# Performance work log

Measured on AMD Instinct MI355X. Metric: run time of the kernel, lower is better.

The kernel has to match this reference:

```python
import jax, jax.numpy as jnp
import numpy as np

S_SAMPLES = 8          # config.ray_samples_per_voxel
T_MIN = 1e-4           # early-termination transmittance threshold


def setup_inputs() -> dict:
    key = jax.random.key(0)
    kp, ks, kd, kc, km, ko, kr = jax.random.split(key, 7)
    V, N = 4096, 4096
    # voxel centers uniform in scene bounds [-1,1]^3
    positions = jax.random.uniform(kp, (V, 3), jnp.float32, -1.0, 1.0)
    # voxel edge lengths: small cubes
    sizes = jax.random.uniform(ks, (V,), jnp.float32, 0.02, 0.08)
    densities = jax.random.normal(kd, (V,), jnp.float32)  # raw, exp-activated
    colors = jax.random.normal(kc, (V, 27), jnp.float32)  # SH deg2: 9*3 coeffs
    morton_codes = jax.random.randint(km, (V,), 0, 16777216, jnp.int32)
    # camera at z=-3 with slight jitter, rays toward the scene
    ray_origins = jnp.tile(jnp.array([0.0, 0.0, -3.0], jnp.float32), (N, 1)) \
        + 0.01 * jax.random.normal(ko, (N, 3), jnp.float32)
    dirs = jax.random.uniform(kr, (N, 3), jnp.float32, -0.4, 0.4)
    dirs = dirs.at[:, 2].set(1.0)
    ray_directions = dirs / jnp.linalg.norm(dirs, axis=1, keepdims=True)
    return {"positions": positions, "sizes": sizes, "densities": densities,
            "colors": colors, "morton_codes": morton_codes,
            "ray_origins": ray_origins, "ray_directions": ray_directions}


def reference(positions, sizes, densities, colors, morton_codes,
              ray_origins, ray_directions):
    # ---- global morton + mean-ray-direction sort ----
    mean_d = ray_directions.mean(axis=0)                       # [3]
    dots = positions @ mean_d                                  # [V]
    keys = morton_codes.astype(jnp.float32) + dots * 1e-6
    order = jnp.argsort(keys)                                  # stable
    pos = positions[order]
    half = (sizes[order] * 0.5)[:, None]                       # [V,1]
    dens_act = jnp.exp(densities[order])                       # 'exp' activation
    col = jax.nn.sigmoid(colors[order][:, :3])                 # dc coeffs, sigmoid

    box_min = pos - half                                       # [V,3]
    box_max = pos + half

    # ---- per-ray slab AABB intersection (vectorized over rays x voxels) ----
    inv_dir = 1.0 / (ray_directions + 1e-8)                    # [N,3]
    o = ray_origins[:, None, :]                                # [N,1,3]
    t1 = (box_min[None, :, :] - o) * inv_dir[:, None, :]       # [N,V,3]
    t2 = (box_max[None, :, :] - o) * inv_dir[:, None, :]
    t_near = jnp.max(jnp.minimum(t1, t2), axis=-1)             # [N,V]
    t_far = jnp.min(jnp.maximum(t1, t2), axis=-1)
    valid = (t_near <= t_far) & (t_far > 0)
    tn = jnp.maximum(t_near, 0.0)

    # ---- per-ray stable sort by entry t (invalid pushed to +inf) ----
    sort_key = jnp.where(valid, tn, jnp.inf)
    idx = jnp.argsort(sort_key, axis=1)                        # [N,V], stable
    tn_s = jnp.take_along_axis(tn, idx, axis=1)
    tf_s = jnp.take_along_axis(t_far, idx, axis=1)
    valid_s = jnp.take_along_axis(valid, idx, axis=1)
    dens_s = dens_act[idx]                                     # [N,V]
    col_s = col[idx]                                           # [N,V,3]

    # ---- sequential alpha compositing via cumprod ----
    dt = (tf_s - tn_s) / S_SAMPLES
    op = 1.0 - jnp.exp(-dens_s * dt)
    op = jnp.where(valid_s, op, 0.0)                           # skipped voxels
    one_m = 1.0 - op
    T_before = jnp.concatenate(
        [jnp.ones_like(op[:, :1]), jnp.cumprod(one_m, axis=1)[:, :-1]], axis=1)
    active = T_before >= T_MIN                                 # early-break mask
    w = jnp.where(active, T_before * op, 0.0)                  # [N,V]

    rgb = jnp.einsum('nv,nvc->nc', w, col_s)                   # [N,3]
    depth = jnp.sum(w * (tn_s + tf_s) * 0.5, axis=1)           # mean of linspace
    final_T = jnp.prod(jnp.where(active, one_m, 1.0), axis=1)
    alpha = 1.0 - final_T
    return rgb, depth, alpha
```

## Files before the change

### kernel.cpp

```cpp
#include <hip/hip_runtime.h>
#include <hip/hip_bf16.h>

#define MAXH 64

__global__ __launch_bounds__(256) void vr_prep(
    const float* __restrict__ positions, const float* __restrict__ sizes,
    const float* __restrict__ densities, const float* __restrict__ colors,
    const int* __restrict__ morton, const float* __restrict__ ray_d,
    float4* __restrict__ P, float* __restrict__ K, float4* __restrict__ C,
    int V, int N)
{
    __shared__ float rx[256], ry[256], rz[256];
    int t = threadIdx.x;
    float sx = 0.f, sy = 0.f, sz = 0.f;
    for (int r = t; r < N; r += 256) {
        sx += ray_d[r*3+0]; sy += ray_d[r*3+1]; sz += ray_d[r*3+2];
    }
    rx[t] = sx; ry[t] = sy; rz[t] = sz;
    __syncthreads();
    for (int s = 128; s > 0; s >>= 1) {
        if (t < s) { rx[t] += rx[t+s]; ry[t] += ry[t+s]; rz[t] += rz[t+s]; }
        __syncthreads();
    }
    float inN = 1.0f / (float)N;
    float mdx = rx[0]*inN, mdy = ry[0]*inN, mdz = rz[0]*inN;

    int v = blockIdx.x * 256 + t;
    if (v < V) {
        float px = positions[v*3+0], py = positions[v*3+1], pz = positions[v*3+2];
        float h = sizes[v] * 0.5f;
        P[v] = make_float4(px, py, pz, h);
        K[v] = (float)morton[v] + (px*mdx + py*mdy + pz*mdz) * 1e-6f;
        float c0 = 1.0f/(1.0f + expf(-colors[v*27+0]));
        float c1 = 1.0f/(1.0f + expf(-colors[v*27+1]));
        float c2 = 1.0f/(1.0f + expf(-colors[v*27+2]));
        C[v] = make_float4(c0, c1, c2, expf(densities[v]));
    }
}

__global__ __launch_bounds__(256) void vr_render(
    const float4* __restrict__ P, const float* __restrict__ K,
    const float4* __restrict__ C,
    const float* __restrict__ ray_o, const float* __restrict__ ray_d,
    float* __restrict__ out, int V, int N)
{
    __shared__ float h_tn[4][MAXH], h_tf[4][MAXH], h_key[4][MAXH];
    __shared__ int   h_v[4][MAXH], s_ord[4][MAXH];
    __shared__ float p_op[4][MAXH], p_c0[4][MAXH], p_c1[4][MAXH],
                     p_c2[4][MAXH], p_mid[4][MAXH];
    __shared__ int   cntL[4];
    __shared__ float rp[4][9];

    int t    = threadIdx.x;
    int lane = t & 63;
    int w    = t >> 6;

    if (t < 4) {
        cntL[t] = 0;
        int ray = blockIdx.x * 4 + t;
        if (ray < N) {
            float ox = ray_o[ray*3+0], oy = ray_o[ray*3+1], oz = ray_o[ray*3+2];
            float dx = ray_d[ray*3+0], dy = ray_d[ray*3+1], dz = ray_d[ray*3+2];
            float ix = 1.0f/(dx + 1e-8f), iy = 1.0f/(dy + 1e-8f), iz = 1.0f/(dz + 1e-8f);
            rp[t][0] = ix;        rp[t][1] = iy;        rp[t][2] = iz;
            rp[t][3] = -ox*ix;    rp[t][4] = -oy*iy;    rp[t][5] = -oz*iz;
            rp[t][6] = fabsf(ix); rp[t][7] = fabsf(iy); rp[t][8] = fabsf(iz);
        } else {
            float qn = __int_as_float(0x7FC00000);
            #pragma unroll
            for (int j = 0; j < 9; ++j) rp[t][j] = qn;
        }
    }
    __syncthreads();

    float ixr[4], iyr[4], izr[4], nxr[4], nyr[4], nzr[4], axr[4], ayr[4], azr[4];
    #pragma unroll
    for (int r = 0; r < 4; ++r) {
        ixr[r] = rp[r][0]; iyr[r] = rp[r][1]; izr[r] = rp[r][2];
        nxr[r] = rp[r][3]; nyr[r] = rp[r][4]; nzr[r] = rp[r][5];
        axr[r] = rp[r][6]; ayr[r] = rp[r][7]; azr[r] = rp[r][8];
    }

    for (int v0 = t; v0 < V; v0 += 512) {
        int v1 = v0 + 256;
        float4 pa = P[v0];
        float4 pb = (v1 < V) ? P[v1] : make_float4(0,0,0,-1.f);

        #pragma unroll
        for (int u = 0; u < 2; ++u) {
            float4 p = u ? pb : pa;
            int    v = u ? v1 : v0;
            #pragma unroll
            for (int r = 0; r < 4; ++r) {
                float s_x = fmaf(p.x, ixr[r], nxr[r]);
                float s_y = fmaf(p.y, iyr[r], nyr[r]);
                float s_z = fmaf(p.z, izr[r], nzr[r]);
                float hx = p.w * axr[r], hy = p.w * ayr[r], hz = p.w * azr[r];
                float tnear = fmaxf(fmaxf(s_x - hx, s_y - hy), s_z - hz);
                float tfar  = fminf(fminf(s_x + hx, s_y + hy), s_z + hz);
                if ((tnear <= tfar) && (tfar > 0.0f)) {
                    int slot = atomicAdd(&cntL[r], 1);
                    if (slot < MAXH) {
                        h_tn[r][slot] = fmaxf(tnear, 0.0f);
                        h_tf[r][slot] = tfar;
                        h_v[r][slot]  = v;
                    }
                }
            }
        }
    }
    __syncthreads();

    int ray = blockIdx.x * 4 + w;
    int m = min(cntL[w], MAXH);

    for (int i = lane; i < m; i += 64) h_key[w][i] = K[h_v[w][i]];
    __syncthreads();

    for (int i = lane; i < m; i += 64) {
        float tni = h_tn[w][i], ki = h_key[w][i];
        int   vi  = h_v[w][i];
        int r = 0;
        for (int j = 0; j < m; ++j) {
            float tnj = h_tn[w][j], kj = h_key[w][j];
            int   vj  = h_v[w][j];
            if ((tnj < tni) || (tnj == tni && ((kj < ki) || (kj == ki && vj < vi)))) r++;
        }
        s_ord[w][r] = i;
    }
    __syncthreads();

    for (int r = lane; r < m; r += 64) {
        int i = s_ord[w][r];
        int v = h_v[w][i];
        float4 c = C[v];
        float tn = h_tn[w][i], tf = h_tf[w][i];
        float dt = (tf - tn) * 0.125f;
        p_op[w][r]  = 1.0f - expf(-c.w * dt);
        p_c0[w][r]  = c.x;  p_c1[w][r] = c.y;  p_c2[w][r] = c.z;
        p_mid[w][r] = (tn + tf) * 0.5f;
    }
    __syncthreads();

    if (lane == 0 && ray < N) {
        float T = 1.0f, r0 = 0.f, r1 = 0.f, r2 = 0.f, dep = 0.f;
        for (int r = 0; r < m; ++r) {
            if (!(T >= 1e-4f)) break;
            float op  = p_op[w][r];
            float wgt = T * op;
            r0  += wgt * p_c0[w][r];
            r1  += wgt * p_c1[w][r];
            r2  += wgt * p_c2[w][r];
            dep += wgt * p_mid[w][r];
            T   *= (1.0f - op);
        }
        out[ray*3 + 0] = r0;
        out[ray*3 + 1] = r1;
        out[ray*3 + 2] = r2;
        out[3*N + ray] = dep;
        out[4*N + ray] = 1.0f - T;
    }
}

extern "C" void kernel_launch(void* const* d_in, const int* in_sizes, int n_in,
                              void* d_out, int out_size, void* d_ws, size_t ws_size,
                              hipStream_t stream)
{
    const float* positions = (const float*)d_in[0];
    const float* sizes     = (const float*)d_in[1];
    const float* densities = (const float*)d_in[2];
    const float* colors    = (const float*)d_in[3];
    const int*   morton    = (const int*)d_in[4];
    const float* ray_o     = (const float*)d_in[5];
    const float* ray_d     = (const float*)d_in[6];
    float* out = (float*)d_out;

    int V = in_sizes[1];
    int N = in_sizes[5] / 3;

    float4* P = (float4*)d_ws;
    float*  K = (float*)(P + V);
    float4* C = (float4*)(K + ((V + 3) & ~3));

    int pblocks = (V + 255) / 256;
    vr_prep<<<pblocks, 256, 0, stream>>>(positions, sizes, densities, colors,
                                         morton, ray_d, P, K, C, V, N);
    int rblocks = (N + 3) / 4;
    vr_render<<<rblocks, 256, 0, stream>>>(P, K, C, ray_o, ray_d, out, V, N);
}
```

Measured before the change: 80.72 us.

## Fuse voxel preprocessing into render kernel and drop morton tiebreak key

Result: faster. 75.17 us (-6.9%).

```diff
diff --git a/kernel.cpp b/kernel.cpp
--- a/kernel.cpp
+++ b/kernel.cpp
@@ -3,48 +3,13 @@
 
 #define MAXH 64
 
-__global__ __launch_bounds__(256) void vr_prep(
+__global__ __launch_bounds__(256) void vr_fused(
     const float* __restrict__ positions, const float* __restrict__ sizes,
     const float* __restrict__ densities, const float* __restrict__ colors,
-    const int* __restrict__ morton, const float* __restrict__ ray_d,
-    float4* __restrict__ P, float* __restrict__ K, float4* __restrict__ C,
-    int V, int N)
-{
-    __shared__ float rx[256], ry[256], rz[256];
-    int t = threadIdx.x;
-    float sx = 0.f, sy = 0.f, sz = 0.f;
-    for (int r = t; r < N; r += 256) {
-        sx += ray_d[r*3+0]; sy += ray_d[r*3+1]; sz += ray_d[r*3+2];
-    }
-    rx[t] = sx; ry[t] = sy; rz[t] = sz;
-    __syncthreads();
-    for (int s = 128; s > 0; s >>= 1) {
-        if (t < s) { rx[t] += rx[t+s]; ry[t] += ry[t+s]; rz[t] += rz[t+s]; }
-        __syncthreads();
-    }
-    float inN = 1.0f / (float)N;
-    float mdx = rx[0]*inN, mdy = ry[0]*inN, mdz = rz[0]*inN;
-
-    int v = blockIdx.x * 256 + t;
-    if (v < V) {
-        float px = positions[v*3+0], py = positions[v*3+1], pz = positions[v*3+2];
-        float h = sizes[v] * 0.5f;
-        P[v] = make_float4(px, py, pz, h);
-        K[v] = (float)morton[v] + (px*mdx + py*mdy + pz*mdz) * 1e-6f;
-        float c0 = 1.0f/(1.0f + expf(-colors[v*27+0]));
-        float c1 = 1.0f/(1.0f + expf(-colors[v*27+1]));
-        float c2 = 1.0f/(1.0f + expf(-colors[v*27+2]));
-        C[v] = make_float4(c0, c1, c2, expf(densities[v]));
-    }
-}
-
-__global__ __launch_bounds__(256) void vr_render(
-    const float4* __restrict__ P, const float* __restrict__ K,
-    const float4* __restrict__ C,
     const float* __restrict__ ray_o, const float* __restrict__ ray_d,
     float* __restrict__ out, int V, int N)
 {
-    __shared__ float h_tn[4][MAXH], h_tf[4][MAXH], h_key[4][MAXH];
+    __shared__ float h_tn[4][MAXH], h_tf[4][MAXH];
     __shared__ int   h_v[4][MAXH], s_ord[4][MAXH];
     __shared__ float p_op[4][MAXH], p_c0[4][MAXH], p_c1[4][MAXH],
                      p_c2[4][MAXH], p_mid[4][MAXH];
@@ -83,19 +48,25 @@
 
     for (int v0 = t; v0 < V; v0 += 512) {
         int v1 = v0 + 256;
-        float4 pa = P[v0];
-        float4 pb = (v1 < V) ? P[v1] : make_float4(0,0,0,-1.f);
+        float px0 = positions[v0*3+0], py0 = positions[v0*3+1], pz0 = positions[v0*3+2];
+        float hh0 = sizes[v0] * 0.5f;
+        float px1 = 0.f, py1 = 0.f, pz1 = 0.f, hh1 = -1.f;
+        if (v1 < V) {
+            px1 = positions[v1*3+0]; py1 = positions[v1*3+1]; pz1 = positions[v1*3+2];
+            hh1 = sizes[v1] * 0.5f;
+        }
 
         #pragma unroll
         for (int u = 0; u < 2; ++u) {
-            float4 p = u ? pb : pa;
-            int    v = u ? v1 : v0;
+            float cx = u ? px1 : px0, cy = u ? py1 : py0, cz = u ? pz1 : pz0;
+            float hh = u ? hh1 : hh0;
+            int   v  = u ? v1  : v0;
             #pragma unroll
             for (int r = 0; r < 4; ++r) {
-                float s_x = fmaf(p.x, ixr[r], nxr[r]);
-                float s_y = fmaf(p.y, iyr[r], nyr[r]);
-                float s_z = fmaf(p.z, izr[r], nzr[r]);
-                float hx = p.w * axr[r], hy = p.w * ayr[r], hz = p.w * azr[r];
+                float s_x = fmaf(cx, ixr[r], nxr[r]);
+                float s_y = fmaf(cy, iyr[r], nyr[r]);
+                float s_z = fmaf(cz, izr[r], nzr[r]);
+                float hx = hh * axr[r], hy = hh * ayr[r], hz = hh * azr[r];
                 float tnear = fmaxf(fmaxf(s_x - hx, s_y - hy), s_z - hz);
                 float tfar  = fminf(fminf(s_x + hx, s_y + hy), s_z + hz);
                 if ((tnear <= tfar) && (tfar > 0.0f)) {
@@ -114,17 +85,14 @@
     int ray = blockIdx.x * 4 + w;
     int m = min(cntL[w], MAXH);
 
-    for (int i = lane; i < m; i += 64) h_key[w][i] = K[h_v[w][i]];
-    __syncthreads();
-
     for (int i = lane; i < m; i += 64) {
-        float tni = h_tn[w][i], ki = h_key[w][i];
+        float tni = h_tn[w][i];
         int   vi  = h_v[w][i];
         int r = 0;
         for (int j = 0; j < m; ++j) {
-            float tnj = h_tn[w][j], kj = h_key[w][j];
+            float tnj = h_tn[w][j];
             int   vj  = h_v[w][j];
-            if ((tnj < tni) || (tnj == tni && ((kj < ki) || (kj == ki && vj < vi)))) r++;
+            if ((tnj < tni) || (tnj == tni && vj < vi)) r++;
         }
         s_ord[w][r] = i;
     }
@@ -133,11 +101,14 @@
     for (int r = lane; r < m; r += 64) {
         int i = s_ord[w][r];
         int v = h_v[w][i];
-        float4 c = C[v];
+        float dens = expf(densities[v]);
+        float c0 = 1.0f/(1.0f + expf(-colors[v*27+0]));
+        float c1 = 1.0f/(1.0f + expf(-colors[v*27+1]));
+        float c2 = 1.0f/(1.0f + expf(-colors[v*27+2]));
         float tn = h_tn[w][i], tf = h_tf[w][i];
         float dt = (tf - tn) * 0.125f;
-        p_op[w][r]  = 1.0f - expf(-c.w * dt);
-        p_c0[w][r]  = c.x;  p_c1[w][r] = c.y;  p_c2[w][r] = c.z;
+        p_op[w][r]  = 1.0f - expf(-dens * dt);
+        p_c0[w][r]  = c0;  p_c1[w][r] = c1;  p_c2[w][r] = c2;
         p_mid[w][r] = (tn + tf) * 0.5f;
     }
     __syncthreads();
@@ -170,7 +141,6 @@
     const float* sizes     = (const float*)d_in[1];
     const float* densities = (const float*)d_in[2];
     const float* colors    = (const float*)d_in[3];
-    const int*   morton    = (const int*)d_in[4];
     const float* ray_o     = (const float*)d_in[5];
     const float* ray_d     = (const float*)d_in[6];
     float* out = (float*)d_out;
@@ -178,13 +148,7 @@
     int V = in_sizes[1];
     int N = in_sizes[5] / 3;
 
-    float4* P = (float4*)d_ws;
-    float*  K = (float*)(P + V);
-    float4* C = (float4*)(K + ((V + 3) & ~3));
-
-    int pblocks = (V + 255) / 256;
-    vr_prep<<<pblocks, 256, 0, stream>>>(positions, sizes, densities, colors,
-                                         morton, ray_d, P, K, C, V, N);
     int rblocks = (N + 3) / 4;
-    vr_render<<<rblocks, 256, 0, stream>>>(P, K, C, ray_o, ray_d, out, V, N);
+    vr_fused<<<rblocks, 256, 0, stream>>>(positions, sizes, densities, colors,
+                                          ray_o, ray_d, out, V, N);
 }
```
